# Kernel tuning notes

Measured on AMD Instinct MI355X. Metric: run time of the kernel, lower is better.

Reference implementation:

```python
import jax, jax.numpy as jnp
import numpy as np


def _three_nn(parent_xyz, xyz):
    # parent_xyz: (bs, n, 3) queries; xyz: (bs, m, 3) reference points.
    # Squared pairwise distances (bs, n, m) without forming (x-y)^2 tensor of rank 4.
    d2 = (jnp.sum(parent_xyz**2, -1, keepdims=True)
          - 2.0 * jnp.einsum('bnd,bmd->bnm', parent_xyz, xyz)
          + jnp.sum(xyz**2, -1)[:, None, :])
    neg_d2, idx = jax.lax.top_k(-d2, 3)           # 3 smallest distances
    dist = jnp.sqrt(jnp.maximum(-neg_d2, 0.0))    # pointnet2 returns sqrt(dist2)
    return dist, idx                              # (bs, n, 3), (bs, n, 3)


def _three_interpolate(feats, idx, weight):
    # feats: (bs, c, m); idx, weight: (bs, n, 3) -> (bs, c, n)
    feats_t = jnp.swapaxes(feats, 1, 2)                     # (bs, m, c)
    gathered = jax.vmap(lambda f, i: f[i])(feats_t, idx)    # (bs, n, 3, c)
    out = jnp.einsum('bnkc,bnk->bcn', gathered, weight)
    return out


def _conv1x1(x, W, b):
    # x: (bs, c_in, n); W: (c_out, c_in); b: (c_out,)
    return jnp.einsum('oc,bcn->bon', W, x) + b[None, :, None]


def setup_inputs() -> dict:
    key = jax.random.key(0)
    ks = jax.random.split(key, 6)
    bs, m, n = 8, 1024, 4096
    c0, c1, c2 = 256, 128, 256
    xyz = jax.random.normal(ks[0], (bs, m, 3), jnp.float32)
    parent_xyz = jax.random.normal(ks[1], (bs, n, 3), jnp.float32)
    feats = jax.random.normal(ks[2], (bs, c0, m), jnp.float32)
    skip_feats = jax.random.normal(ks[3], (bs, c1, n), jnp.float32)
    W1 = jax.random.normal(ks[4], (c2, c0 + c1), jnp.float32) * (1.0 / np.sqrt(c0 + c1))
    b1 = jnp.zeros((c2,), jnp.float32)
    W2 = jax.random.normal(ks[5], (c2, c2), jnp.float32) * (1.0 / np.sqrt(c2))
    b2 = jnp.zeros((c2,), jnp.float32)
    return {"xyz": xyz, "parent_xyz": parent_xyz, "feats": feats,
            "skip_feats": skip_feats, "W1": W1, "b1": b1, "W2": W2, "b2": b2}


def reference(xyz, parent_xyz, feats, skip_feats, W1, b1, W2, b2):
    dist, idx = _three_nn(parent_xyz, xyz)
    inv_dist = 1.0 / (dist + 1e-8)
    weight = inv_dist / jnp.sum(inv_dist, 2, keepdims=True)     # (bs, n, 3)
    up_feats = _three_interpolate(feats, idx, weight)           # (bs, c0, n)
    parent_feats = jnp.concatenate([up_feats, skip_feats], 1)   # (bs, c0+c1, n)
    h = jax.nn.relu(_conv1x1(parent_feats, W1, b1))
    out = jax.nn.relu(_conv1x1(h, W2, b2))
    return out
```

## Files before the change

### kernel.cpp

```cpp
#include <hip/hip_runtime.h>
#include <hip/hip_bf16.h>
#include <cstddef>
#include <cstdint>

#define BS    8
#define M_PTS 1024
#define N_PTS 4096
#define C0    256
#define C1    128
#define C2    256
#define K1DIM 384

typedef __attribute__((ext_vector_type(8))) short bf16x8;
typedef __attribute__((ext_vector_type(4))) float f32x4;

__device__ __forceinline__ ushort f2bf(float f) {
  union { float f; unsigned u; } v; v.f = f;
  unsigned r = v.u + 0x7fffu + ((v.u >> 16) & 1u);
  return (ushort)(r >> 16);
}

__device__ __forceinline__ float rdlane_f(float v, int lane) {
  union { float f; int i; } u; u.f = v;
  u.i = __builtin_amdgcn_readlane(u.i, lane);
  return u.f;
}

__global__ __launch_bounds__(256) void prep_k(
    const float* __restrict__ feats, const float* __restrict__ W1,
    const float* __restrict__ W2, float* __restrict__ featsT,
    ushort* __restrict__ W1f, ushort* __restrict__ W2f) {
  __shared__ float tile[32][33];
  const int t = threadIdx.x;
  if (blockIdx.x < 2048) {
    const int bx = blockIdx.x & 31;
    const int by = (blockIdx.x >> 5) & 7;
    const int bz = blockIdx.x >> 8;
    const int tx = t & 31, ty = t >> 5;
    const float* ip = feats + (size_t)bz * C0 * M_PTS;
    float*       op = featsT + (size_t)bz * C0 * M_PTS;
    const int r0 = by * 32, c0 = bx * 32;
#pragma unroll
    for (int i = 0; i < 4; ++i)
      tile[ty + i * 8][tx] = ip[(size_t)(r0 + ty + i * 8) * M_PTS + c0 + tx];
    __syncthreads();
#pragma unroll
    for (int i = 0; i < 4; ++i)
      op[(size_t)(c0 + ty + i * 8) * C0 + r0 + tx] = tile[tx][ty + i * 8];
  } else {
    const int id = (blockIdx.x - 2048) * 256 + t;
    if (id < C2 * K1DIM) {
      int m = id / K1DIM, k = id - m * K1DIM;
      int off = (((m >> 4) * 12 + (k >> 5)) * 4 + ((k >> 3) & 3)) * 128 + (m & 15) * 8 + (k & 7);
      W1f[off] = f2bf(W1[id]);
    }
    if (id < C2 * C2) {
      int m = id >> 8, k = id & 255;
      int off = (((m >> 4) * 8 + (k >> 5)) * 4 + ((k >> 3) & 3)) * 128 + (m & 15) * 8 + (k & 7);
      W2f[off] = f2bf(W2[id]);
    }
  }
}

__global__ __launch_bounds__(256, 4) void fp_fused_k(
    const float* __restrict__ xyz,
    const float* __restrict__ pxyz,
    const float* __restrict__ featsT,
    const float* __restrict__ skip,
    const ushort* __restrict__ W1f,
    const float* __restrict__ b1,
    const ushort* __restrict__ W2f,
    const float* __restrict__ b2,
    float* __restrict__ out) {
  __shared__ float4 smemq[2560];
  float4* pts4 = smemq;
  ushort* pfB  = (ushort*)(smemq + 1024);
  ushort* hbuf = (ushort*)smemq;

  const int t  = threadIdx.x;
  const int b  = blockIdx.x & 7;
  const int n0 = (blockIdx.x >> 3) * 32;
  const int wv = t >> 6, l = t & 63;
  const int q  = t >> 3, sub = t & 7;

  const float qx = pxyz[((size_t)b * N_PTS + n0 + q) * 3 + 0];
  const float qy = pxyz[((size_t)b * N_PTS + n0 + q) * 3 + 1];
  const float qz = pxyz[((size_t)b * N_PTS + n0 + q) * 3 + 2];

#pragma unroll
  for (int it = 0; it < 4; ++it) {
    const int m = t + it * 256;
    const float x = xyz[(size_t)b * 3 * M_PTS + 3 * m + 0];
    const float y = xyz[(size_t)b * 3 * M_PTS + 3 * m + 1];
    const float z = xyz[(size_t)b * 3 * M_PTS + 3 * m + 2];
    const float s2 = __fadd_rn(__fadd_rn(__fmul_rn(x, x), __fmul_rn(y, y)),
                               __fmul_rn(z, z));
    pts4[m ^ ((m >> 7) & 7)] = (float4){x, y, z, s2};
  }

  float skp[16];
#pragma unroll
  for (int it = 0; it < 8; ++it) {
    const int id = t + it * 256;
    const int r2 = id >> 5, nn = id & 31;
    skp[2 * it + 0] = skip[((size_t)b * C1 + 2 * r2 + 0) * N_PTS + n0 + nn];
    skp[2 * it + 1] = skip[((size_t)b * C1 + 2 * r2 + 1) * N_PTS + n0 + nn];
  }

  const float qq = __fadd_rn(__fadd_rn(__fmul_rn(qx, qx), __fmul_rn(qy, qy)),
                             __fmul_rn(qz, qz));
  __syncthreads();

  float d0 = 3.4e38f, d1 = 3.4e38f, d2 = 3.4e38f;
  int   i0 = 0, i1 = 0, i2 = 0;
  {
    const float4* pblk = pts4 + sub * 128;
    int off[8];
#pragma unroll
    for (int e = 0; e < 8; ++e) off[e] = e ^ sub;
    const int mbase = sub * 128;
    for (int a = 0; a < 16; ++a) {
      const int mb = mbase + (a << 3);
#pragma unroll
      for (int e = 0; e < 8; ++e) {
        const float4 P = pblk[(a << 3) + off[e]];
        const float dot = __fadd_rn(__fadd_rn(__fmul_rn(qx, P.x), __fmul_rn(qy, P.y)),
                                    __fmul_rn(qz, P.z));
        const float d = __fadd_rn(__fsub_rn(qq, __fmul_rn(2.0f, dot)), P.w);
        const int m = mb + e;
        const bool c0 = d < d0, c1 = d < d1, c2 = d < d2;
        i2 = c1 ? i1 : (c2 ? m : i2);
        i1 = c0 ? i0 : (c1 ? m : i1);
        i0 = c0 ? m : i0;
        d2 = __builtin_amdgcn_fmed3f(d, d1, d2);
        d1 = __builtin_amdgcn_fmed3f(d, d0, d1);
        d0 = fminf(d, d0);
      }
    }
  }

#pragma unroll
  for (int mk = 1; mk <= 4; mk <<= 1) {
    const float pd0 = __shfl_xor(d0, mk), pd1 = __shfl_xor(d1, mk), pd2 = __shfl_xor(d2, mk);
    const int   pi0 = __shfl_xor(i0, mk), pi1 = __shfl_xor(i1, mk), pi2 = __shfl_xor(i2, mk);
    const bool lo = (sub & mk) == 0;
    const float a0 = lo ? d0 : pd0, a1 = lo ? d1 : pd1, a2 = lo ? d2 : pd2;
    const float b0 = lo ? pd0 : d0, b1v = lo ? pd1 : d1, b2v = lo ? pd2 : d2;
    const int   A0 = lo ? i0 : pi0, A1 = lo ? i1 : pi1, A2 = lo ? i2 : pi2;
    const int   B0 = lo ? pi0 : i0, B1 = lo ? pi1 : i1, B2 = lo ? pi2 : i2;
    const bool c0 = b0 < a0;
    const bool cb1a0 = b1v < a0, cb0a1 = b0 < a1;
    const bool cb1a1 = b1v < a1, cb2a0 = b2v < a0, cb0a2 = b0 < a2;
    const float m0 = c0 ? b0 : a0;                 const int M0 = c0 ? B0 : A0;
    const float t1a = cb1a0 ? b1v : a0;            const int T1a = cb1a0 ? B1 : A0;
    const float t1b = cb0a1 ? b0 : a1;             const int T1b = cb0a1 ? B0 : A1;
    const float m1 = c0 ? t1a : t1b;               const int M1 = c0 ? T1a : T1b;
    const float sA = cb2a0 ? b2v : a0;             const int SA = cb2a0 ? B2 : A0;
    const float sB = cb1a1 ? b1v : a1;             const int SB = cb1a1 ? B1 : A1;
    const float sD = cb0a2 ? b0 : a2;              const int SD = cb0a2 ? B0 : A2;
    const float m2 = c0 ? (cb1a0 ? sA : sB) : (cb0a1 ? sB : sD);
    const int   M2 = c0 ? (cb1a0 ? SA : SB) : (cb0a1 ? SB : SD);
    d0 = m0; d1 = m1; d2 = m2; i0 = M0; i1 = M1; i2 = M2;
  }

  float w0f, w1f, w2f;
  {
    const float t0 = sqrtf(fmaxf(d0, 0.f)), t1 = sqrtf(fmaxf(d1, 0.f)),
                t2 = sqrtf(fmaxf(d2, 0.f));
    const float r0 = 1.0f / (t0 + 1e-8f), r1 = 1.0f / (t1 + 1e-8f),
                r2 = 1.0f / (t2 + 1e-8f);
    const float rs = __fadd_rn(__fadd_rn(r0, r1), r2);
    w0f = r0 / rs; w1f = r1 / rs; w2f = r2 / rs;
  }

  {
    const float* fb = featsT + (size_t)b * M_PTS * C0;
#pragma unroll
    for (int qi = 0; qi < 8; ++qi) {
      const int src = qi * 8;
      const int  j0 = __builtin_amdgcn_readlane(i0, src);
      const int  j1 = __builtin_amdgcn_readlane(i1, src);
      const int  j2 = __builtin_amdgcn_readlane(i2, src);
      const float w0 = rdlane_f(w0f, src), w1 = rdlane_f(w1f, src), w2 = rdlane_f(w2f, src);
      const float4 f0 = *(const float4*)(fb + (size_t)j0 * C0 + l * 4);
      const float4 f1 = *(const float4*)(fb + (size_t)j1 * C0 + l * 4);
      const float4 f2 = *(const float4*)(fb + (size_t)j2 * C0 + l * 4);
      ushort4 hv;
      hv.x = f2bf(w0 * f0.x + w1 * f1.x + w2 * f2.x);
      hv.y = f2bf(w0 * f0.y + w1 * f1.y + w2 * f2.y);
      hv.z = f2bf(w0 * f0.z + w1 * f1.z + w2 * f2.z);
      hv.w = f2bf(w0 * f0.w + w1 * f1.w + w2 * f2.w);
      const int nq = wv * 8 + qi;
      const int kq = l >> 1;
      const int u = kq * 32 + (nq ^ (kq & 7));
      *reinterpret_cast<ushort4*>(&pfB[u * 8 + (l & 1) * 4]) = hv;
    }
  }
#pragma unroll
  for (int it = 0; it < 8; ++it) {
    const int id = t + it * 256;
    const int r2 = id >> 5, nn = id & 31;
    const int k = C0 + 2 * r2;
    const int kq = k >> 3;
    const int u = kq * 32 + (nn ^ (kq & 7));
    ushort2 sv; sv.x = f2bf(skp[2 * it]); sv.y = f2bf(skp[2 * it + 1]);
    *reinterpret_cast<ushort2*>(&pfB[u * 8 + (k & 7)]) = sv;
  }
  __syncthreads();

  const int c = l & 15, g = l >> 4;

  f32x4 acc[4][2];
#pragma unroll
  for (int i = 0; i < 4; ++i)
#pragma unroll
    for (int j = 0; j < 2; ++j) acc[i][j] = (f32x4){0.f, 0.f, 0.f, 0.f};

  for (int kb = 0; kb < 12; ++kb) {
    const int kqg = kb * 4 + g;
    bf16x8 bfr[2], afr[4];
#pragma unroll
    for (int j = 0; j < 2; ++j)
      bfr[j] = *reinterpret_cast<const bf16x8*>(&pfB[(kqg * 32 + ((j * 16 + c) ^ (kqg & 7))) * 8]);
#pragma unroll
    for (int i = 0; i < 4; ++i)
      afr[i] = *reinterpret_cast<const bf16x8*>(&W1f[(((wv * 4 + i) * 12 + kb) * 4 + g) * 128 + c * 8]);
    __builtin_amdgcn_s_setprio(1);
#pragma unroll
    for (int i = 0; i < 4; ++i)
#pragma unroll
      for (int j = 0; j < 2; ++j)
        acc[i][j] = __builtin_amdgcn_mfma_f32_16x16x32_bf16(afr[i], bfr[j], acc[i][j], 0, 0, 0);
    __builtin_amdgcn_s_setprio(0);
  }

#pragma unroll
  for (int i = 0; i < 4; ++i) {
    const int mbase = wv * 64 + i * 16 + g * 4;
    const float4 bias = *(const float4*)(b1 + mbase);
#pragma unroll
    for (int j = 0; j < 2; ++j) {
      const int nn = j * 16 + c;
      const int kq = mbase >> 3;
      const int u = kq * 32 + (nn ^ (kq & 7));
      ushort4 hv;
      hv.x = f2bf(fmaxf(acc[i][j].x + bias.x, 0.f));
      hv.y = f2bf(fmaxf(acc[i][j].y + bias.y, 0.f));
      hv.z = f2bf(fmaxf(acc[i][j].z + bias.z, 0.f));
      hv.w = f2bf(fmaxf(acc[i][j].w + bias.w, 0.f));
      *reinterpret_cast<ushort4*>(&hbuf[u * 8 + (mbase & 7)]) = hv;
    }
  }
  __syncthreads();

#pragma unroll
  for (int i = 0; i < 4; ++i)
#pragma unroll
    for (int j = 0; j < 2; ++j) acc[i][j] = (f32x4){0.f, 0.f, 0.f, 0.f};

  for (int kb = 0; kb < 8; ++kb) {
    const int kqg = kb * 4 + g;
    bf16x8 bfr[2], afr[4];
#pragma unroll
    for (int j = 0; j < 2; ++j)
      bfr[j] = *reinterpret_cast<const bf16x8*>(&hbuf[(kqg * 32 + ((j * 16 + c) ^ (kqg & 7))) * 8]);
#pragma unroll
    for (int i = 0; i < 4; ++i)
      afr[i] = *reinterpret_cast<const bf16x8*>(&W2f[(((wv * 4 + i) * 8 + kb) * 4 + g) * 128 + c * 8]);
    __builtin_amdgcn_s_setprio(1);
#pragma unroll
    for (int i = 0; i < 4; ++i)
#pragma unroll
      for (int j = 0; j < 2; ++j)
        acc[i][j] = __builtin_amdgcn_mfma_f32_16x16x32_bf16(afr[i], bfr[j], acc[i][j], 0, 0, 0);
    __builtin_amdgcn_s_setprio(0);
  }

#pragma unroll
  for (int i = 0; i < 4; ++i) {
    const int mbase = wv * 64 + i * 16 + g * 4;
    const float4 bias = *(const float4*)(b2 + mbase);
#pragma unroll
    for (int j = 0; j < 2; ++j) {
      const int nn = n0 + j * 16 + c;
      out[((size_t)b * C2 + mbase + 0) * N_PTS + nn] = fmaxf(acc[i][j].x + bias.x, 0.f);
      out[((size_t)b * C2 + mbase + 1) * N_PTS + nn] = fmaxf(acc[i][j].y + bias.y, 0.f);
      out[((size_t)b * C2 + mbase + 2) * N_PTS + nn] = fmaxf(acc[i][j].z + bias.z, 0.f);
      out[((size_t)b * C2 + mbase + 3) * N_PTS + nn] = fmaxf(acc[i][j].w + bias.w, 0.f);
    }
  }
}

extern "C" void kernel_launch(void* const* d_in, const int* in_sizes, int n_in,
                              void* d_out, int out_size, void* d_ws, size_t ws_size,
                              hipStream_t stream) {
  const float* xyz   = (const float*)d_in[0];
  const float* pxyz  = (const float*)d_in[1];
  const float* feats = (const float*)d_in[2];
  const float* skip  = (const float*)d_in[3];
  const float* W1    = (const float*)d_in[4];
  const float* b1    = (const float*)d_in[5];
  const float* W2    = (const float*)d_in[6];
  const float* b2    = (const float*)d_in[7];
  float* out = (float*)d_out;

  float*  ws     = (float*)d_ws;
  float*  featsT = ws;
  ushort* W1f    = (ushort*)(featsT + (size_t)BS * M_PTS * C0);
  ushort* W2f    = W1f + (size_t)C2 * K1DIM;

  prep_k<<<2432, 256, 0, stream>>>(feats, W1, W2, featsT, W1f, W2f);
  fp_fused_k<<<BS * (N_PTS / 32), 256, 0, stream>>>(xyz, pxyz, featsT, skip,
                                                    W1f, b1, W2f, b2, out);
}
```

Before: 46.82 us.

## Double query tile to 64 per 512-thread block and pack distance math

Each block now handles 64 query points with 512 threads instead of 32 with 256. This halves the per-query cost of staging reference points into LDS and of fetching weights, and reshapes each wave's MFMA tiles to 32 output channels by 64 points. The reference points are stored in a paired SoA layout so the distance computation uses packed v_pk_mul/v_pk_add FP32 instructions on two candidates at a time. An extra barrier separates the GEMM1 reads from the hbuf writes, which now alias the point buffer. In exchange, LDS use grows to 64KB per block, which may reduce occupancy, and the grid has half as many blocks.

```diff
diff --git a/kernel.cpp b/kernel.cpp
--- a/kernel.cpp
+++ b/kernel.cpp
@@ -13,6 +13,7 @@
 
 typedef __attribute__((ext_vector_type(8))) short bf16x8;
 typedef __attribute__((ext_vector_type(4))) float f32x4;
+typedef __attribute__((ext_vector_type(2))) float f32x2;
 
 __device__ __forceinline__ ushort f2bf(float f) {
   union { float f; unsigned u; } v; v.f = f;
@@ -24,6 +25,13 @@
   union { float f; int i; } u; u.f = v;
   u.i = __builtin_amdgcn_readlane(u.i, lane);
   return u.f;
+}
+
+__device__ __forceinline__ f32x2 pk_mul(f32x2 a, f32x2 b) {
+  f32x2 r; asm("v_pk_mul_f32 %0, %1, %2" : "=v"(r) : "v"(a), "v"(b)); return r;
+}
+__device__ __forceinline__ f32x2 pk_add(f32x2 a, f32x2 b) {
+  f32x2 r; asm("v_pk_add_f32 %0, %1, %2" : "=v"(r) : "v"(a), "v"(b)); return r;
 }
 
 __global__ __launch_bounds__(256) void prep_k(
@@ -62,7 +70,7 @@
   }
 }
 
-__global__ __launch_bounds__(256, 4) void fp_fused_k(
+__global__ __launch_bounds__(512, 4) void fp_fused_k(
     const float* __restrict__ xyz,
     const float* __restrict__ pxyz,
     const float* __restrict__ featsT,
@@ -72,14 +80,14 @@
     const ushort* __restrict__ W2f,
     const float* __restrict__ b2,
     float* __restrict__ out) {
-  __shared__ float4 smemq[2560];
+  __shared__ float4 smemq[4096];
   float4* pts4 = smemq;
-  ushort* pfB  = (ushort*)(smemq + 1024);
+  ushort* pfB  = (ushort*)smemq + 8192;
   ushort* hbuf = (ushort*)smemq;
 
   const int t  = threadIdx.x;
   const int b  = blockIdx.x & 7;
-  const int n0 = (blockIdx.x >> 3) * 32;
+  const int n0 = (blockIdx.x >> 3) * 64;
   const int wv = t >> 6, l = t & 63;
   const int q  = t >> 3, sub = t & 7;
 
@@ -87,22 +95,24 @@
   const float qy = pxyz[((size_t)b * N_PTS + n0 + q) * 3 + 1];
   const float qz = pxyz[((size_t)b * N_PTS + n0 + q) * 3 + 2];
 
-#pragma unroll
-  for (int it = 0; it < 4; ++it) {
-    const int m = t + it * 256;
-    const float x = xyz[(size_t)b * 3 * M_PTS + 3 * m + 0];
-    const float y = xyz[(size_t)b * 3 * M_PTS + 3 * m + 1];
-    const float z = xyz[(size_t)b * 3 * M_PTS + 3 * m + 2];
-    const float s2 = __fadd_rn(__fadd_rn(__fmul_rn(x, x), __fmul_rn(y, y)),
-                               __fmul_rn(z, z));
-    pts4[m ^ ((m >> 7) & 7)] = (float4){x, y, z, s2};
+  {
+    const float2* xb = (const float2*)(xyz + (size_t)b * 3 * M_PTS + 6 * t);
+    const float2 A = xb[0], B = xb[1], C = xb[2];
+    const float x0 = A.x, y0 = A.y, z0 = B.x, x1 = B.y, y1 = C.x, z1 = C.y;
+    const float s0 = __fadd_rn(__fadd_rn(__fmul_rn(x0, x0), __fmul_rn(y0, y0)),
+                               __fmul_rn(z0, z0));
+    const float s1 = __fadd_rn(__fadd_rn(__fmul_rn(x1, x1), __fmul_rn(y1, y1)),
+                               __fmul_rn(z1, z1));
+    const int U = t ^ ((t >> 6) & 7);
+    pts4[U * 2 + 0] = (float4){x0, x1, y0, y1};
+    pts4[U * 2 + 1] = (float4){z0, z1, s0, s1};
   }
 
   float skp[16];
 #pragma unroll
   for (int it = 0; it < 8; ++it) {
-    const int id = t + it * 256;
-    const int r2 = id >> 5, nn = id & 31;
+    const int id = t + it * 512;
+    const int r2 = id >> 6, nn = id & 63;
     skp[2 * it + 0] = skip[((size_t)b * C1 + 2 * r2 + 0) * N_PTS + n0 + nn];
     skp[2 * it + 1] = skip[((size_t)b * C1 + 2 * r2 + 1) * N_PTS + n0 + nn];
   }
@@ -114,29 +124,44 @@
   float d0 = 3.4e38f, d1 = 3.4e38f, d2 = 3.4e38f;
   int   i0 = 0, i1 = 0, i2 = 0;
   {
-    const float4* pblk = pts4 + sub * 128;
-    int off[8];
-#pragma unroll
-    for (int e = 0; e < 8; ++e) off[e] = e ^ sub;
-    const int mbase = sub * 128;
-    for (int a = 0; a < 16; ++a) {
-      const int mb = mbase + (a << 3);
+    const f32x2 Qx2 = {qx, qx}, Qy2 = {qy, qy}, Qz2 = {qz, qz};
+    const f32x2 Qq2 = {qq, qq}, Mn2 = {-2.0f, -2.0f};
+    int pe[8];
+#pragma unroll
+    for (int e = 0; e < 8; ++e) pe[e] = (sub * 64 + (e ^ sub)) * 2;
+    for (int jb = 0; jb < 8; ++jb) {
 #pragma unroll
       for (int e = 0; e < 8; ++e) {
-        const float4 P = pblk[(a << 3) + off[e]];
-        const float dot = __fadd_rn(__fadd_rn(__fmul_rn(qx, P.x), __fmul_rn(qy, P.y)),
-                                    __fmul_rn(qz, P.z));
-        const float d = __fadd_rn(__fsub_rn(qq, __fmul_rn(2.0f, dot)), P.w);
-        const int m = mb + e;
-        const bool c0 = d < d0, c1 = d < d1, c2 = d < d2;
-        i2 = c1 ? i1 : (c2 ? m : i2);
-        i1 = c0 ? i0 : (c1 ? m : i1);
-        i0 = c0 ? m : i0;
-        d2 = __builtin_amdgcn_fmed3f(d, d1, d2);
-        d1 = __builtin_amdgcn_fmed3f(d, d0, d1);
-        d0 = fminf(d, d0);
+        const float4 lo = pts4[pe[e] + jb * 16];
+        const float4 hi = pts4[pe[e] + jb * 16 + 1];
+        const f32x2 Xp = {lo.x, lo.y}, Yp = {lo.z, lo.w};
+        const f32x2 Zp = {hi.x, hi.y}, Sp = {hi.z, hi.w};
+        const f32x2 dotp = pk_add(pk_add(pk_mul(Qx2, Xp), pk_mul(Qy2, Yp)),
+                                  pk_mul(Qz2, Zp));
+        const f32x2 dp = pk_add(pk_add(Qq2, pk_mul(dotp, Mn2)), Sp);
+        {
+          const float d = dp.x; const int m = jb * 16 + 2 * e;
+          const bool c0 = d < d0, c1 = d < d1, c2 = d < d2;
+          i2 = c1 ? i1 : (c2 ? m : i2);
+          i1 = c0 ? i0 : (c1 ? m : i1);
+          i0 = c0 ? m : i0;
+          d2 = __builtin_amdgcn_fmed3f(d, d1, d2);
+          d1 = __builtin_amdgcn_fmed3f(d, d0, d1);
+          d0 = fminf(d, d0);
+        }
+        {
+          const float d = dp.y; const int m = jb * 16 + 2 * e + 1;
+          const bool c0 = d < d0, c1 = d < d1, c2 = d < d2;
+          i2 = c1 ? i1 : (c2 ? m : i2);
+          i1 = c0 ? i0 : (c1 ? m : i1);
+          i0 = c0 ? m : i0;
+          d2 = __builtin_amdgcn_fmed3f(d, d1, d2);
+          d1 = __builtin_amdgcn_fmed3f(d, d0, d1);
+          d0 = fminf(d, d0);
+        }
       }
     }
+    i0 += sub * 128; i1 += sub * 128; i2 += sub * 128;
   }
 
 #pragma unroll
@@ -192,96 +217,97 @@
       hv.w = f2bf(w0 * f0.w + w1 * f1.w + w2 * f2.w);
       const int nq = wv * 8 + qi;
       const int kq = l >> 1;
-      const int u = kq * 32 + (nq ^ (kq & 7));
-      *reinterpret_cast<ushort4*>(&pfB[u * 8 + (l & 1) * 4]) = hv;
+      *reinterpret_cast<ushort4*>(
+          &pfB[(kq * 64 + (nq ^ (kq & 7))) * 8 + (l & 1) * 4]) = hv;
     }
   }
 #pragma unroll
   for (int it = 0; it < 8; ++it) {
-    const int id = t + it * 256;
-    const int r2 = id >> 5, nn = id & 31;
+    const int id = t + it * 512;
+    const int r2 = id >> 6, nn = id & 63;
     const int k = C0 + 2 * r2;
     const int kq = k >> 3;
-    const int u = kq * 32 + (nn ^ (kq & 7));
     ushort2 sv; sv.x = f2bf(skp[2 * it]); sv.y = f2bf(skp[2 * it + 1]);
-    *reinterpret_cast<ushort2*>(&pfB[u * 8 + (k & 7)]) = sv;
+    *reinterpret_cast<ushort2*>(
+        &pfB[(kq * 64 + (nn ^ (kq & 7))) * 8 + (k & 7)]) = sv;
   }
   __syncthreads();
 
   const int c = l & 15, g = l >> 4;
 
-  f32x4 acc[4][2];
-#pragma unroll
-  for (int i = 0; i < 4; ++i)
-#pragma unroll
-    for (int j = 0; j < 2; ++j) acc[i][j] = (f32x4){0.f, 0.f, 0.f, 0.f};
+  f32x4 acc[2][4];
+#pragma unroll
+  for (int i = 0; i < 2; ++i)
+#pragma unroll
+    for (int j = 0; j < 4; ++j) acc[i][j] = (f32x4){0.f, 0.f, 0.f, 0.f};
 
   for (int kb = 0; kb < 12; ++kb) {
     const int kqg = kb * 4 + g;
-    bf16x8 bfr[2], afr[4];
-#pragma unroll
-    for (int j = 0; j < 2; ++j)
-      bfr[j] = *reinterpret_cast<const bf16x8*>(&pfB[(kqg * 32 + ((j * 16 + c) ^ (kqg & 7))) * 8]);
-#pragma unroll
-    for (int i = 0; i < 4; ++i)
-      afr[i] = *reinterpret_cast<const bf16x8*>(&W1f[(((wv * 4 + i) * 12 + kb) * 4 + g) * 128 + c * 8]);
+    bf16x8 bfr[4], afr[2];
+#pragma unroll
+    for (int j = 0; j < 4; ++j)
+      bfr[j] = *reinterpret_cast<const bf16x8*>(&pfB[(kqg * 64 + ((j * 16 + c) ^ (kqg & 7))) * 8]);
+#pragma unroll
+    for (int i = 0; i < 2; ++i)
+      afr[i] = *reinterpret_cast<const bf16x8*>(&W1f[(((wv * 2 + i) * 12 + kb) * 4 + g) * 128 + c * 8]);
     __builtin_amdgcn_s_setprio(1);
 #pragma unroll
-    for (int i = 0; i < 4; ++i)
-#pragma unroll
-      for (int j = 0; j < 2; ++j)
+    for (int i = 0; i < 2; ++i)
+#pragma unroll
+      for (int j = 0; j < 4; ++j)
         acc[i][j] = __builtin_amdgcn_mfma_f32_16x16x32_bf16(afr[i], bfr[j], acc[i][j], 0, 0, 0);
     __builtin_amdgcn_s_setprio(0);
   }
-
-#pragma unroll
-  for (int i = 0; i < 4; ++i) {
-    const int mbase = wv * 64 + i * 16 + g * 4;
+  __syncthreads();
+
+#pragma unroll
+  for (int i = 0; i < 2; ++i) {
+    const int mbase = wv * 32 + i * 16 + g * 4;
     const float4 bias = *(const float4*)(b1 + mbase);
 #pragma unroll
-    for (int j = 0; j < 2; ++j) {
+    for (int j = 0; j < 4; ++j) {
       const int nn = j * 16 + c;
       const int kq = mbase >> 3;
-      const int u = kq * 32 + (nn ^ (kq & 7));
       ushort4 hv;
       hv.x = f2bf(fmaxf(acc[i][j].x + bias.x, 0.f));
       hv.y = f2bf(fmaxf(acc[i][j].y + bias.y, 0.f));
       hv.z = f2bf(fmaxf(acc[i][j].z + bias.z, 0.f));
       hv.w = f2bf(fmaxf(acc[i][j].w + bias.w, 0.f));
-      *reinterpret_cast<ushort4*>(&hbuf[u * 8 + (mbase & 7)]) = hv;
+      *reinterpret_cast<ushort4*>(
+          &hbuf[(kq * 64 + (nn ^ (kq & 7))) * 8 + (mbase & 7)]) = hv;
     }
   }
   __syncthreads();
 
 #pragma unroll
-  for (int i = 0; i < 4; ++i)
-#pragma unroll
-    for (int j = 0; j < 2; ++j) acc[i][j] = (f32x4){0.f, 0.f, 0.f, 0.f};
+  for (int i = 0; i < 2; ++i)
+#pragma unroll
+    for (int j = 0; j < 4; ++j) acc[i][j] = (f32x4){0.f, 0.f, 0.f, 0.f};
 
   for (int kb = 0; kb < 8; ++kb) {
     const int kqg = kb * 4 + g;
-    bf16x8 bfr[2], afr[4];
-#pragma unroll
-    for (int j = 0; j < 2; ++j)
-      bfr[j] = *reinterpret_cast<const bf16x8*>(&hbuf[(kqg * 32 + ((j * 16 + c) ^ (kqg & 7))) * 8]);
-#pragma unroll
-    for (int i = 0; i < 4; ++i)
-      afr[i] = *reinterpret_cast<const bf16x8*>(&W2f[(((wv * 4 + i) * 8 + kb) * 4 + g) * 128 + c * 8]);
+    bf16x8 bfr[4], afr[2];
+#pragma unroll
+    for (int j = 0; j < 4; ++j)
+      bfr[j] = *reinterpret_cast<const bf16x8*>(&hbuf[(kqg * 64 + ((j * 16 + c) ^ (kqg & 7))) * 8]);
+#pragma unroll
+    for (int i = 0; i < 2; ++i)
+      afr[i] = *reinterpret_cast<const bf16x8*>(&W2f[(((wv * 2 + i) * 8 + kb) * 4 + g) * 128 + c * 8]);
     __builtin_amdgcn_s_setprio(1);
 #pragma unroll
-    for (int i = 0; i < 4; ++i)
-#pragma unroll
-      for (int j = 0; j < 2; ++j)
+    for (int i = 0; i < 2; ++i)
+#pragma unroll
+      for (int j = 0; j < 4; ++j)
         acc[i][j] = __builtin_amdgcn_mfma_f32_16x16x32_bf16(afr[i], bfr[j], acc[i][j], 0, 0, 0);
     __builtin_amdgcn_s_setprio(0);
   }
 
 #pragma unroll
-  for (int i = 0; i < 4; ++i) {
-    const int mbase = wv * 64 + i * 16 + g * 4;
+  for (int i = 0; i < 2; ++i) {
+    const int mbase = wv * 32 + i * 16 + g * 4;
     const float4 bias = *(const float4*)(b2 + mbase);
 #pragma unroll
-    for (int j = 0; j < 2; ++j) {
+    for (int j = 0; j < 4; ++j) {
       const int nn = n0 + j * 16 + c;
       out[((size_t)b * C2 + mbase + 0) * N_PTS + nn] = fmaxf(acc[i][j].x + bias.x, 0.f);
       out[((size_t)b * C2 + mbase + 1) * N_PTS + nn] = fmaxf(acc[i][j].y + bias.y, 0.f);
@@ -310,6 +336,6 @@
   ushort* W2f    = W1f + (size_t)C2 * K1DIM;
 
   prep_k<<<2432, 256, 0, stream>>>(feats, W1, W2, featsT, W1f, W2f);
-  fp_fused_k<<<BS * (N_PTS / 32), 256, 0, stream>>>(xyz, pxyz, featsT, skip,
+  fp_fused_k<<<BS * (N_PTS / 64), 512, 0, stream>>>(xyz, pxyz, featsT, skip,
                                                     W1f, b1, W2f, b2, out);
 }
```

Measured after the change: 47.49 us. About the same (+1.4%).
